# Performance work log

Hardware: AMD Instinct MI355X
Metric: run time of the kernel (lower is better)

The kernel has to match this reference:

```python
import jax, jax.numpy as jnp
import numpy as np

DIM = 512
HEADS = 8
DIM_HEAD = 64
INNER = HEADS * DIM_HEAD  # 512


def setup_inputs() -> dict:
    key = jax.random.key(0)
    k1, k2, k3, k4 = jax.random.split(key, 4)
    x = jax.random.normal(k1, (2, 2048, DIM), dtype=jnp.float32)
    # nn.Linear weights are [out_features, in_features]
    w_qkv = jax.random.normal(k2, (INNER * 3, DIM), dtype=jnp.float32) * (1.0 / np.sqrt(DIM))
    w_out = jax.random.normal(k3, (DIM, INNER), dtype=jnp.float32) * (1.0 / np.sqrt(INNER))
    b_out = jax.random.normal(k4, (DIM,), dtype=jnp.float32) * 0.01
    return {"x": x, "w_qkv": w_qkv, "w_out": w_out, "b_out": b_out}


def reference(x, w_qkv, w_out, b_out):
    b, n, _ = x.shape
    qkv = x @ w_qkv.T  # (b, n, 3*inner)
    q, k, v = jnp.split(qkv, 3, axis=-1)
    # (b, n, inner) -> (b, h, n, dh)
    def to_heads(t):
        return t.reshape(b, n, HEADS, DIM_HEAD).transpose(0, 2, 1, 3)
    q, k, v = map(to_heads, (q, k, v))
    # Faithful to the torch code: softmax over head dim for q, over seq for k
    q = jax.nn.softmax(q, axis=-1)
    k = jax.nn.softmax(k, axis=-2)
    # torch einsum labels seq as i/j, head dim as d (contracted) -> [n, n] context
    context = jnp.einsum('bhid,bhjd->bhij', k, v)     # (b, h, n, n)
    out = jnp.einsum('bhij,bhie->bhje', context, q)   # (b, h, n, dh)
    out = out.transpose(0, 2, 1, 3).reshape(b, n, INNER)
    return out @ w_out.T + b_out
```

## Files before the change

### kernel.cpp

```cpp
#include <hip/hip_runtime.h>
#include <hip/hip_bf16.h>
#include <math.h>

#define BB   2
#define NN   2048
#define DIMM 512
#define HH   8
#define NC3  1536
#define BN   4096

typedef __attribute__((ext_vector_type(8))) short short8;
typedef __attribute__((ext_vector_type(4))) float f32x4;
typedef unsigned short u16t;

__device__ inline short bfc(float f) {
    __hip_bfloat16 h = __float2bfloat16(f);
    return *reinterpret_cast<short*>(&h);
}
__device__ inline float bf2f(u16t u) {
    return __uint_as_float(((unsigned)u) << 16);
}

#define SWZ(P) ((P) ^ ((((P) >> 7) & 3) << 4))

__device__ inline void gll16(const u16t* gp, void* lp) {
    __builtin_amdgcn_global_load_lds(
        (const __attribute__((address_space(1))) void*)gp,
        (__attribute__((address_space(3))) void*)lp,
        16, 0, 0);
}

__global__ __launch_bounds__(256) void cvt_bf16(
    const float* __restrict__ x, const float* __restrict__ wq,
    u16t* __restrict__ xb, u16t* __restrict__ wqb)
{
    int t = blockIdx.x * 256 + threadIdx.x;
    const float4* src; ushort4* dst; int i;
    if (t < 524288) { src = (const float4*)x;  dst = (ushort4*)xb;  i = t; }
    else            { src = (const float4*)wq; dst = (ushort4*)wqb; i = t - 524288; }
    float4 v = src[i];
    ushort4 u;
    u.x = (u16t)bfc(v.x); u.y = (u16t)bfc(v.y);
    u.z = (u16t)bfc(v.z); u.w = (u16t)bfc(v.w);
    dst[i] = u;
}

__global__ __launch_bounds__(256) void qkvgemm(
    const u16t* __restrict__ A, const u16t* __restrict__ Bw,
    u16t* __restrict__ QKV)
{
    __shared__ __align__(16) char smem[32768];

    const int tid  = threadIdx.x;
    const int wave = tid >> 6, lane = tid & 63;
    const int wr = wave >> 1, wc = wave & 1;

    int bid = blockIdx.y * gridDim.x + blockIdx.x;
    int swz = (bid & 7) * 48 + (bid >> 3);
    const int row0 = (swz & 31) * 128;
    const int c0   = (swz >> 5) * 128;

    size_t gA[2], gB[2];
#pragma unroll
    for (int j = 0; j < 2; ++j) {
        int c = wave * 2 + j;
        int X = (c * 64 + lane) * 16;
        int gi = SWZ(X) >> 4;
        int row = gi >> 2, col = (gi & 3) * 8;
        gA[j] = (size_t)(row0 + row) * DIMM + col;
        gB[j] = (size_t)(c0   + row) * DIMM + col;
    }

    int rdA[4], rdB[4];
#pragma unroll
    for (int i = 0; i < 4; ++i) {
        int Pa = (wr * 64 + i * 16 + (lane & 15)) * 64 + (lane >> 4) * 16;
        rdA[i] = SWZ(Pa);
        int Pb = (wc * 64 + i * 16 + (lane & 15)) * 64 + (lane >> 4) * 16;
        rdB[i] = 8192 + SWZ(Pb);
    }

#define QSTAGE(BUF, KT) {                                                     \
    char* sb = smem + (BUF) * 16384;                                          \
    _Pragma("unroll")                                                         \
    for (int j = 0; j < 2; ++j) {                                             \
        gll16(A  + gA[j] + (KT), sb + (wave * 2 + j) * 1024);                 \
        gll16(Bw + gB[j] + (KT), sb + 8192 + (wave * 2 + j) * 1024);          \
    } }

    f32x4 acc[4][4];
#pragma unroll
    for (int i = 0; i < 4; ++i)
#pragma unroll
        for (int j = 0; j < 4; ++j) acc[i][j] = (f32x4){0.f, 0.f, 0.f, 0.f};

    QSTAGE(0, 0);
    for (int t = 0; t < 16; ++t) {
        __syncthreads();
        if (t < 15) QSTAGE((t + 1) & 1, (t + 1) * 32);
        const char* rb = smem + (t & 1) * 16384;
        short8 af[4], bfr[4];
#pragma unroll
        for (int i = 0; i < 4; ++i) {
            af[i]  = *(const short8*)(rb + rdA[i]);
            bfr[i] = *(const short8*)(rb + rdB[i]);
        }
#pragma unroll
        for (int i = 0; i < 4; ++i)
#pragma unroll
            for (int j = 0; j < 4; ++j)
                acc[i][j] = __builtin_amdgcn_mfma_f32_16x16x32_bf16(
                    af[i], bfr[j], acc[i][j], 0, 0, 0);
    }
#undef QSTAGE

#pragma unroll
    for (int j = 0; j < 4; ++j) {
        int col = c0 + wc * 64 + j * 16 + (lane & 15);
#pragma unroll
        for (int i = 0; i < 4; ++i) {
#pragma unroll
            for (int r = 0; r < 4; ++r) {
                int row = row0 + wr * 64 + i * 16 + (lane >> 4) * 4 + r;
                QKV[(size_t)row * NC3 + col] = (u16t)bfc(acc[i][j][r]);
            }
        }
    }
}

#define TST 136

__global__ __launch_bounds__(512) void mpart(
    const u16t* __restrict__ QKV, float* __restrict__ Mp, float* __restrict__ ksump)
{
    __shared__ __align__(16) char sh[34816];
    u16t* ksT = (u16t*)sh;
    u16t* qsT = (u16t*)(sh + 17408);

    const int bh = blockIdx.x, ch = blockIdx.y;
    const int b = bh >> 3, h = bh & 7;
    const int tid = threadIdx.x;
    const u16t* base = QKV + ((size_t)b * NN + ch * 128) * NC3 + h * 64;

    const int k7 = tid & 7;
    const int d0 = k7 * 8;
    const int rr = tid >> 3;

#pragma unroll
    for (int pass = 0; pass < 2; ++pass) {
        int r = pass * 64 + rr;
        const u16t* rowp = base + (size_t)r * NC3 + d0;
        short8 qv = *(const short8*)(rowp);
        short8 kv = *(const short8*)(rowp + 512);
        float e[8]; float s = 0.f;
#pragma unroll
        for (int u = 0; u < 8; ++u) { e[u] = __expf(bf2f((u16t)qv[u])); s += e[u]; }
        s += __shfl_xor(s, 1); s += __shfl_xor(s, 2); s += __shfl_xor(s, 4);
        float inv = 1.0f / s;
        int gx = ((r >> 3) ^ k7) * 8 + (r & 7);
#pragma unroll
        for (int u = 0; u < 8; ++u)
            qsT[(d0 + u) * TST + gx] = (u16t)bfc(e[u] * inv);
#pragma unroll
        for (int u = 0; u < 8; ++u)
            ksT[(d0 + u) * TST + gx] = (u16t)bfc(__expf(bf2f((u16t)kv[u])));
    }
    __syncthreads();

    if (tid < 64) {
        float kss = 0.f;
#pragma unroll
        for (int gg = 0; gg < 16; ++gg) {
            short8 v = *(const short8*)(ksT + tid * TST + gg * 8);
#pragma unroll
            for (int u = 0; u < 8; ++u) kss += bf2f((u16t)v[u]);
        }
        ksump[(bh * 16 + ch) * 64 + tid] = kss;
    }

    const int wave = tid >> 6, lane = tid & 63;
    const int g = wave >> 1, kh = wave & 1;
    const int dl = lane & 15, kq = lane >> 4;
    const int d = g * 16 + dl;

    f32x4 acc[4];
#pragma unroll
    for (int j = 0; j < 4; ++j) acc[j] = (f32x4){0.f, 0.f, 0.f, 0.f};

#pragma unroll
    for (int ks2 = 0; ks2 < 2; ++ks2) {
        int kb = kh * 64 + ks2 * 32 + kq * 8;
        short8 af = *(const short8*)(ksT + d * TST + ((((kb >> 3) ^ (d >> 3))) << 3));
#pragma unroll
        for (int j = 0; j < 4; ++j) {
            int e = j * 16 + dl;
            short8 bfrj = *(const short8*)(qsT + e * TST + ((((kb >> 3) ^ (e >> 3))) << 3));
            acc[j] = __builtin_amdgcn_mfma_f32_16x16x32_bf16(af, bfrj, acc[j], 0, 0, 0);
        }
    }

    float* mp = Mp + ((size_t)((bh * 16 + ch) * 2 + kh)) * 4096;
#pragma unroll
    for (int j = 0; j < 4; ++j)
#pragma unroll
        for (int r = 0; r < 4; ++r)
            mp[(g * 16 + kq * 4 + r) * 64 + j * 16 + dl] = acc[j][r];
}

__global__ __launch_bounds__(256) void w2t(
    const float* __restrict__ Mp, const float* __restrict__ ksump,
    const float* __restrict__ w_out, u16t* __restrict__ W2T)
{
    __shared__ float kst[64];
    __shared__ float Ms[64][68];
    __shared__ float Wt[64][68];

    int bh = blockIdx.x, ot = blockIdx.y;
    int b = bh >> 3, h = bh & 7;
    int tid = threadIdx.x;
    int d = tid & 63, og = tid >> 6;

    if (tid < 64) {
        float s = 0.f;
#pragma unroll
        for (int c = 0; c < 16; ++c) s += ksump[(bh * 16 + c) * 64 + tid];
        kst[tid] = s;
    }
    for (int idx = tid; idx < 4096; idx += 256) {
        const float* p = Mp + (size_t)bh * 32 * 4096 + idx;
        float s = 0.f;
#pragma unroll
        for (int c = 0; c < 32; ++c) s += p[c * 4096];
        Ms[idx >> 6][idx & 63] = s;
    }
    {
        int o = tid >> 2, e0 = (tid & 3) * 16;
#pragma unroll
        for (int q = 0; q < 4; ++q)
            *(float4*)&Wt[o][e0 + q * 4] =
                *(const float4*)&w_out[(size_t)(ot * 64 + o) * DIMM + h * 64 + e0 + q * 4];
    }
    __syncthreads();

    float Mreg[64];
#pragma unroll
    for (int e4 = 0; e4 < 16; ++e4) {
        float4 v = *(const float4*)&Ms[d][e4 * 4];
        Mreg[e4 * 4 + 0] = v.x; Mreg[e4 * 4 + 1] = v.y;
        Mreg[e4 * 4 + 2] = v.z; Mreg[e4 * 4 + 3] = v.w;
    }
    float inv = 1.0f / kst[d];

#pragma unroll
    for (int oo = 0; oo < 16; ++oo) {
        int o = og * 16 + oo;
        float a = 0.f;
#pragma unroll
        for (int e4 = 0; e4 < 16; ++e4) {
            float4 wv = *(const float4*)&Wt[o][e4 * 4];
            a += wv.x * Mreg[e4 * 4 + 0] + wv.y * Mreg[e4 * 4 + 1]
               + wv.z * Mreg[e4 * 4 + 2] + wv.w * Mreg[e4 * 4 + 3];
        }
        W2T[((size_t)b * DIMM + ot * 64 + o) * DIMM + h * 64 + d] = (u16t)bfc(a * inv);
    }
}

__global__ __launch_bounds__(256) void outgemm(
    const u16t* __restrict__ Aq, const u16t* __restrict__ W2T,
    const float* __restrict__ bias, float* __restrict__ Out)
{
    __shared__ __align__(16) char smem[24576];

    const int tid  = threadIdx.x;
    const int wave = tid >> 6, lane = tid & 63;
    const int wr = wave >> 1, wc = wave & 1;

    int bid = blockIdx.y * gridDim.x + blockIdx.x;
    int swz = (bid & 7) * 32 + (bid >> 3);
    const int row0 = (swz & 31) * 128;
    const int c0   = (swz >> 5) * 64;
    const u16t* Bp = W2T + (size_t)(row0 >> 11) * (DIMM * DIMM);

    size_t gA[2], gB;
#pragma unroll
    for (int j = 0; j < 2; ++j) {
        int c = wave * 2 + j;
        int gi = SWZ((c * 64 + lane) * 16) >> 4;
        int row = gi >> 2, col = (gi & 3) * 8;
        gA[j] = (size_t)(row0 + row) * NC3 + col;
    }
    {
        int gi = SWZ((wave * 64 + lane) * 16) >> 4;
        int row = gi >> 2, col = (gi & 3) * 8;
        gB = (size_t)(c0 + row) * DIMM + col;
    }

    int rdA[4], rdB[2];
#pragma unroll
    for (int i = 0; i < 4; ++i) {
        int Pa = (wr * 64 + i * 16 + (lane & 15)) * 64 + (lane >> 4) * 16;
        rdA[i] = SWZ(Pa);
    }
#pragma unroll
    for (int j = 0; j < 2; ++j) {
        int Pb = (wc * 32 + j * 16 + (lane & 15)) * 64 + (lane >> 4) * 16;
        rdB[j] = 8192 + SWZ(Pb);
    }

#define OSTAGE(BUF, KT) {                                                     \
    char* sb = smem + (BUF) * 12288;                                          \
    _Pragma("unroll")                                                         \
    for (int j = 0; j < 2; ++j)                                               \
        gll16(Aq + gA[j] + (KT), sb + (wave * 2 + j) * 1024);                 \
    gll16(Bp + gB + (KT), sb + 8192 + wave * 1024);                           \
    }

    f32x4 acc[4][2];
#pragma unroll
    for (int i = 0; i < 4; ++i)
#pragma unroll
        for (int j = 0; j < 2; ++j) acc[i][j] = (f32x4){0.f, 0.f, 0.f, 0.f};

    OSTAGE(0, 0);
    for (int t = 0; t < 16; ++t) {
        __syncthreads();
        if (t < 15) OSTAGE((t + 1) & 1, (t + 1) * 32);
        const char* rb = smem + (t & 1) * 12288;
        short8 af[4], bfr[2];
#pragma unroll
        for (int i = 0; i < 4; ++i) af[i]  = *(const short8*)(rb + rdA[i]);
#pragma unroll
        for (int j = 0; j < 2; ++j) bfr[j] = *(const short8*)(rb + rdB[j]);
#pragma unroll
        for (int i = 0; i < 4; ++i)
#pragma unroll
            for (int j = 0; j < 2; ++j)
                acc[i][j] = __builtin_amdgcn_mfma_f32_16x16x32_bf16(
                    af[i], bfr[j], acc[i][j], 0, 0, 0);
    }
#undef OSTAGE

#pragma unroll
    for (int j = 0; j < 2; ++j) {
        int col = c0 + wc * 32 + j * 16 + (lane & 15);
        float bb = bias[col];
#pragma unroll
        for (int i = 0; i < 4; ++i) {
#pragma unroll
            for (int r = 0; r < 4; ++r) {
                int row = row0 + wr * 64 + i * 16 + (lane >> 4) * 4 + r;
                Out[(size_t)row * DIMM + col] = acc[i][j][r] + bb;
            }
        }
    }
}

extern "C" void kernel_launch(void* const* d_in, const int* in_sizes, int n_in,
                              void* d_out, int out_size, void* d_ws, size_t ws_size,
                              hipStream_t stream)
{
    const float* x     = (const float*)d_in[0];
    const float* w_qkv = (const float*)d_in[1];
    const float* w_out = (const float*)d_in[2];
    const float* b_out = (const float*)d_in[3];
    float* out = (float*)d_out;

    char* w = (char*)d_ws;
    u16t*  xb   = (u16t*) (w);
    u16t*  wqb  = (u16t*) (w + 4194304);
    u16t*  QKV  = (u16t*) (w + 5767168);
    float* Mp   = (float*)(w + 18350080);
    float* ksum = (float*)(w + 26738688);
    u16t*  W2T  = (u16t*) (w + 26804224);

    cvt_bf16<<<dim3(2816), 256, 0, stream>>>(x, w_qkv, xb, wqb);

    qkvgemm<<<dim3(32, 12), 256, 0, stream>>>(xb, wqb, QKV);

    mpart<<<dim3(16, 16), 512, 0, stream>>>(QKV, Mp, ksum);

    w2t<<<dim3(16, 8), 256, 0, stream>>>(Mp, ksum, w_out, W2T);

    outgemm<<<dim3(32, 8), 256, 0, stream>>>(QKV + 1024, W2T, b_out, out);
}
```

Baseline: 57.33 us.

## Split partial-context reduction into its own kernel and remap GEMM tile order

Adds an mreduce kernel that sums the 32 partial M matrices per batch-head into a compact buffer, spread across 256 blocks. Before, each of the 128 w2t blocks redid that same 32-way reduction over the same head slice, repeating it eight times. The qkv and output GEMMs now use 1D grids with a new block-to-tile mapping meant to improve L2 reuse. The price is one more kernel launch and an extra round trip through global memory for M.

```diff
diff --git a/kernel.cpp b/kernel.cpp
--- a/kernel.cpp
+++ b/kernel.cpp
@@ -55,10 +55,9 @@
     const int wave = tid >> 6, lane = tid & 63;
     const int wr = wave >> 1, wc = wave & 1;
 
-    int bid = blockIdx.y * gridDim.x + blockIdx.x;
-    int swz = (bid & 7) * 48 + (bid >> 3);
-    const int row0 = (swz & 31) * 128;
-    const int c0   = (swz >> 5) * 128;
+    int bid = blockIdx.x;
+    const int row0 = ((bid & 7) * 4 + ((bid >> 3) & 3)) * 128;
+    const int c0   = (bid >> 5) * 128;
 
     size_t gA[2], gB[2];
 #pragma unroll
@@ -207,8 +206,20 @@
             mp[(g * 16 + kq * 4 + r) * 64 + j * 16 + dl] = acc[j][r];
 }
 
+__global__ __launch_bounds__(256) void mreduce(
+    const float* __restrict__ Mp, float* __restrict__ M)
+{
+    int bh = blockIdx.x;
+    int idx = blockIdx.y * 256 + threadIdx.x;
+    const float* p = Mp + (size_t)bh * 32 * 4096 + idx;
+    float s = 0.f;
+#pragma unroll
+    for (int c = 0; c < 32; ++c) s += p[c * 4096];
+    M[(size_t)bh * 4096 + idx] = s;
+}
+
 __global__ __launch_bounds__(256) void w2t(
-    const float* __restrict__ Mp, const float* __restrict__ ksump,
+    const float* __restrict__ M, const float* __restrict__ ksump,
     const float* __restrict__ w_out, u16t* __restrict__ W2T)
 {
     __shared__ float kst[64];
@@ -226,13 +237,8 @@
         for (int c = 0; c < 16; ++c) s += ksump[(bh * 16 + c) * 64 + tid];
         kst[tid] = s;
     }
-    for (int idx = tid; idx < 4096; idx += 256) {
-        const float* p = Mp + (size_t)bh * 32 * 4096 + idx;
-        float s = 0.f;
-#pragma unroll
-        for (int c = 0; c < 32; ++c) s += p[c * 4096];
-        Ms[idx >> 6][idx & 63] = s;
-    }
+    for (int idx = tid; idx < 4096; idx += 256)
+        Ms[idx >> 6][idx & 63] = M[(size_t)bh * 4096 + idx];
     {
         int o = tid >> 2, e0 = (tid & 3) * 16;
 #pragma unroll
@@ -275,10 +281,9 @@
     const int wave = tid >> 6, lane = tid & 63;
     const int wr = wave >> 1, wc = wave & 1;
 
-    int bid = blockIdx.y * gridDim.x + blockIdx.x;
-    int swz = (bid & 7) * 32 + (bid >> 3);
-    const int row0 = (swz & 31) * 128;
-    const int c0   = (swz >> 5) * 64;
+    int bid = blockIdx.x;
+    const int row0 = ((bid & 7) * 4 + ((bid >> 3) & 3)) * 128;
+    const int c0   = (bid >> 5) * 64;
     const u16t* Bp = W2T + (size_t)(row0 >> 11) * (DIMM * DIMM);
 
     size_t gA[2], gB;
@@ -371,15 +376,18 @@
     u16t*  QKV  = (u16t*) (w + 5767168);
     float* Mp   = (float*)(w + 18350080);
     float* ksum = (float*)(w + 26738688);
-    u16t*  W2T  = (u16t*) (w + 26804224);
+    float* Mm   = (float*)(w + 26804224);
+    u16t*  W2T  = (u16t*) (w + 27066368);
 
     cvt_bf16<<<dim3(2816), 256, 0, stream>>>(x, w_qkv, xb, wqb);
 
-    qkvgemm<<<dim3(32, 12), 256, 0, stream>>>(xb, wqb, QKV);
+    qkvgemm<<<dim3(384), 256, 0, stream>>>(xb, wqb, QKV);
 
     mpart<<<dim3(16, 16), 512, 0, stream>>>(QKV, Mp, ksum);
 
-    w2t<<<dim3(16, 8), 256, 0, stream>>>(Mp, ksum, w_out, W2T);
-
-    outgemm<<<dim3(32, 8), 256, 0, stream>>>(QKV + 1024, W2T, b_out, out);
-}
+    mreduce<<<dim3(16, 16), 256, 0, stream>>>(Mp, Mm);
+
+    w2t<<<dim3(16, 8), 256, 0, stream>>>(Mm, ksum, w_out, W2T);
+
+    outgemm<<<dim3(256), 256, 0, stream>>>(QKV + 1024, W2T, b_out, out);
+}
```

New measurement: 48.86 us. -14.8%, faster.
